# Performance work log

Hardware: AMD Instinct MI355X
Metric: run time of the kernel (lower is better)

## Reference

```python
import jax, jax.numpy as jnp
import numpy as np

NEG_SLOPE = 0.2  # PyG GATConv default negative_slope


def gat_conv(x, edge_index, W, a_src, a_dst, bias, heads, out_ch, concat):
    """PyG-style GATConv (eval mode, add_self_loops=True).
    x: [N, F_in], edge_index: [2, E] (row 0 = src, row 1 = dst).
    """
    N = x.shape[0]
    loop = jnp.arange(N, dtype=edge_index.dtype)
    src = jnp.concatenate([edge_index[0], loop])  # [E+N]
    dst = jnp.concatenate([edge_index[1], loop])

    h = (x @ W).reshape(N, heads, out_ch)            # [N, H, C]
    alpha_s = jnp.einsum('nhc,hc->nh', h, a_src)     # [N, H]
    alpha_d = jnp.einsum('nhc,hc->nh', h, a_dst)

    e = jax.nn.leaky_relu(alpha_s[src] + alpha_d[dst], NEG_SLOPE)  # [E+N, H]
    # softmax over incoming edges per destination node (numerically stable)
    m = jax.ops.segment_max(e, dst, num_segments=N)                # [N, H]
    ex = jnp.exp(e - m[dst])
    denom = jax.ops.segment_sum(ex, dst, num_segments=N)
    alpha = ex / (denom[dst] + 1e-16)                              # [E+N, H]

    msg = h[src] * alpha[:, :, None]                               # [E+N, H, C]
    out = jax.ops.segment_sum(msg, dst, num_segments=N)            # [N, H, C]
    out = out.reshape(N, heads * out_ch) if concat else out.mean(axis=1)
    return out + bias


def setup_inputs() -> dict:
    key = jax.random.key(0)
    ks = jax.random.split(key, 10)
    N, F_in, H, C1, LAT, E = 10000, 2000, 10, 128, 64, 150000
    hid = H * C1  # 1280
    x = jax.random.normal(ks[0], (N, F_in), dtype=jnp.float32)
    edge_index = jax.random.randint(ks[1], (2, E), 0, N, dtype=jnp.int64)
    # layer 1 params (glorot-ish scaling)
    W1 = jax.random.normal(ks[2], (F_in, H * C1), dtype=jnp.float32) * (1.0 / np.sqrt(F_in))
    a_src1 = jax.random.normal(ks[3], (H, C1), dtype=jnp.float32) * 0.1
    a_dst1 = jax.random.normal(ks[4], (H, C1), dtype=jnp.float32) * 0.1
    b1 = jnp.zeros((hid,), dtype=jnp.float32)
    # layer 2 params
    W2 = jax.random.normal(ks[5], (hid, H * LAT), dtype=jnp.float32) * (1.0 / np.sqrt(hid))
    a_src2 = jax.random.normal(ks[6], (H, LAT), dtype=jnp.float32) * 0.1
    a_dst2 = jax.random.normal(ks[7], (H, LAT), dtype=jnp.float32) * 0.1
    b2 = jnp.zeros((LAT,), dtype=jnp.float32)
    return {"x": x, "edge_index": edge_index,
            "W1": W1, "a_src1": a_src1, "a_dst1": a_dst1, "b1": b1,
            "W2": W2, "a_src2": a_src2, "a_dst2": a_dst2, "b2": b2}


def reference(x, edge_index, W1, a_src1, a_dst1, b1, W2, a_src2, a_dst2, b2):
    H, C1, LAT = 10, 128, 64
    h1 = gat_conv(x, edge_index, W1, a_src1, a_dst1, b1, H, C1, concat=True)
    h1 = jax.nn.relu(h1)
    h2 = gat_conv(h1, edge_index, W2, a_src2, a_dst2, b2, H, LAT, concat=False)
    return jax.nn.relu(h2)
```

## Files before the change

### kernel.cpp

```cpp
#include <hip/hip_runtime.h>

#define NN    10000
#define FIN   2000
#define NH    10
#define C1    128
#define C2    64
#define HC1   1280
#define HC2   640
#define MP    10240
#define K1P   2016

typedef _Float16 f16x8 __attribute__((ext_vector_type(8)));
typedef _Float16 f16x4 __attribute__((ext_vector_type(4)));
typedef _Float16 f16x2 __attribute__((ext_vector_type(2)));
typedef float    f32x4 __attribute__((ext_vector_type(4)));

__device__ __forceinline__ float leaky(float x) { return x > 0.f ? x : 0.2f * x; }

__global__ void k_cast_count(const float* __restrict__ src, _Float16* __restrict__ dst,
                             int R, int C4, int Cp4,
                             const int* __restrict__ ei, int* __restrict__ counts, int E) {
    if (blockIdx.x == 1) {
        int e = blockIdx.y * 256 + threadIdx.x;
        if (e < E) atomicAdd(&counts[ei[E + e]], 1);
    }
    int c = blockIdx.x * 256 + threadIdx.x;
    int r = blockIdx.y;
    if (c >= Cp4) return;
    float4 v = make_float4(0.f, 0.f, 0.f, 0.f);
    if (r < R && c < C4) v = *(const float4*)(src + (long)r * (C4 * 4) + 4 * c);
    f16x4 o = {(_Float16)v.x, (_Float16)v.y, (_Float16)v.z, (_Float16)v.w};
    *(f16x4*)(dst + (long)r * (Cp4 * 4) + 4 * c) = o;
}

__global__ void k_transpose_both(const float* __restrict__ W1, _Float16* __restrict__ W1t,
                                 const float* __restrict__ W2, _Float16* __restrict__ W2t,
                                 int* __restrict__ counts) {
    __shared__ float tile[32][33];
    if (blockIdx.x == 0) {
        int i = blockIdx.y * 256 + threadIdx.x;
        if (i <= NN) counts[i] = 0;
    }
    const float* W; _Float16* Wt; int K, N, Kpad, kbase, nbase;
    if (blockIdx.y < 40) {
        W = W1; Wt = W1t; K = FIN; N = HC1; Kpad = K1P;
        kbase = blockIdx.x * 32; nbase = blockIdx.y * 32;
    } else {
        if (blockIdx.x >= 40) return;
        W = W2; Wt = W2t; K = HC1; N = HC2; Kpad = HC1;
        kbase = blockIdx.x * 32; nbase = (blockIdx.y - 40) * 32;
        if (nbase >= N) return;
    }
    int tx = threadIdx.x & 31;
    int ty = threadIdx.x >> 5;
#pragma unroll
    for (int i = 0; i < 4; i++) {
        int k = kbase + ty + i * 8;
        float v = (k < K) ? W[(long)k * N + nbase + tx] : 0.0f;
        tile[ty + i * 8][tx] = v;
    }
    __syncthreads();
#pragma unroll
    for (int i = 0; i < 4; i++) {
        int n = nbase + ty + i * 8;
        Wt[(long)n * Kpad + kbase + tx] = (_Float16)tile[tx][ty + i * 8];
    }
}

__device__ __forceinline__ void gl2lds16(const void* g, void* l) {
    __builtin_amdgcn_global_load_lds((const __attribute__((address_space(1))) void*)g,
                                     (__attribute__((address_space(3))) void*)l, 16, 0, 0);
}

#define WAITCNT_VM6  0x0F76
#define WAITCNT_VM0  0x0F70

__global__ __launch_bounds__(256, 2) void k_gemm(const _Float16* __restrict__ A,
                                                 const _Float16* __restrict__ Bt,
                                                 _Float16* __restrict__ C, int K, int N,
                                                 int NTN,
                                                 const float* __restrict__ asf,
                                                 const float* __restrict__ adf,
                                                 float* __restrict__ as,
                                                 float* __restrict__ ad,
                                                 int headw) {
    __shared__ char smem[73728] __attribute__((aligned(16)));
    _Float16* As = (_Float16*)smem;
    _Float16* Bs = (_Float16*)(smem + 49152);

    int bid = blockIdx.x;
    int r = bid & 7, qb = bid >> 3;
    int n_t = qb % NTN;
    int m_t = r + 8 * (qb / NTN);
    int m0 = m_t * 256;
    int n0 = n_t * 128;
    int t = threadIdx.x;
    int lane = t & 63, wave = t >> 6;
    int wr = wave >> 1, wc = wave & 1;
    int lrow = lane & 15, q = lane >> 4;

    f32x4 acc[8][4] = {};

    int sA[4], sB[2];
#pragma unroll
    for (int i = 0; i < 4; i++) sA[i] = t + 256 * i;
#pragma unroll
    for (int i = 0; i < 2; i++) sB[i] = t + 256 * i;
    const _Float16* Ar[4];
    const _Float16* Br[2];
#pragma unroll
    for (int i = 0; i < 4; i++) {
        int row = sA[i] >> 2, gq = (sA[i] & 3) ^ ((sA[i] >> 3) & 3);
        Ar[i] = A + (long)(m0 + row) * K + gq * 8;
    }
#pragma unroll
    for (int i = 0; i < 2; i++) {
        int row = sB[i] >> 2, gq = (sB[i] & 3) ^ ((sB[i] >> 3) & 3);
        Br[i] = Bt + (long)(n0 + row) * K + gq * 8;
    }

    int aoff[8], boff[4];
#pragma unroll
    for (int i = 0; i < 8; i++) {
        int rowa = wr * 128 + i * 16 + lrow;
        aoff[i] = rowa * 32 + ((q ^ ((rowa >> 1) & 3)) << 3);
    }
#pragma unroll
    for (int i = 0; i < 4; i++) {
        int rowb = wc * 64 + i * 16 + lrow;
        boff[i] = rowb * 32 + ((q ^ ((rowb >> 1) & 3)) << 3);
    }

    auto stage = [&](int it, int buf) {
        int k0 = it << 5;
#pragma unroll
        for (int i = 0; i < 4; i++) gl2lds16(Ar[i] + k0, &As[buf * 8192 + sA[i] * 8]);
#pragma unroll
        for (int i = 0; i < 2; i++) gl2lds16(Br[i] + k0, &Bs[buf * 4096 + sB[i] * 8]);
    };

    int nk = K >> 5;
    stage(0, 0);
    stage(1, 1);
    int cur = 0;
    for (int it = 0; it < nk; it++) {
        if (it + 1 < nk) __builtin_amdgcn_s_waitcnt(WAITCNT_VM6);
        else             __builtin_amdgcn_s_waitcnt(WAITCNT_VM0);
        __builtin_amdgcn_s_barrier();
        int nxt = cur + 2; if (nxt >= 3) nxt -= 3;
        if (it + 2 < nk) stage(it + 2, nxt);

        f16x8 af[8], bf[4];
#pragma unroll
        for (int i = 0; i < 8; i++) af[i] = *(const f16x8*)&As[cur * 8192 + aoff[i]];
#pragma unroll
        for (int i = 0; i < 4; i++) bf[i] = *(const f16x8*)&Bs[cur * 4096 + boff[i]];
#pragma unroll
        for (int mt = 0; mt < 8; mt++)
#pragma unroll
            for (int nt = 0; nt < 4; nt++)
                acc[mt][nt] = __builtin_amdgcn_mfma_f32_16x16x32_f16(bf[nt], af[mt], acc[mt][nt], 0, 0, 0);
        cur = (cur + 1 == 3) ? 0 : cur + 1;
    }

#pragma unroll
    for (int mt = 0; mt < 8; mt++) {
        int m = m0 + wr * 128 + mt * 16 + lrow;
#pragma unroll
        for (int nt = 0; nt < 4; nt++) {
            int n = n0 + wc * 64 + nt * 16 + q * 4;
            f16x4 o = {(_Float16)acc[mt][nt][0], (_Float16)acc[mt][nt][1],
                       (_Float16)acc[mt][nt][2], (_Float16)acc[mt][nt][3]};
            *(f16x4*)(C + (long)m * N + n) = o;
        }
    }

    float4 av[4], dvv[4];
#pragma unroll
    for (int nt = 0; nt < 4; nt++) {
        av[nt]  = *(const float4*)(asf + n0 + wc * 64 + nt * 16 + q * 4);
        dvv[nt] = *(const float4*)(adf + n0 + wc * 64 + nt * 16 + q * 4);
    }
    __syncthreads();
    float* sAs = (float*)smem;
    float* sAd = (float*)smem + 512;
#pragma unroll
    for (int mt = 0; mt < 8; mt++) {
        float ps = 0.f, pd = 0.f;
#pragma unroll
        for (int nt = 0; nt < 4; nt++) {
            ps += acc[mt][nt][0] * av[nt].x + acc[mt][nt][1] * av[nt].y
                + acc[mt][nt][2] * av[nt].z + acc[mt][nt][3] * av[nt].w;
            pd += acc[mt][nt][0] * dvv[nt].x + acc[mt][nt][1] * dvv[nt].y
                + acc[mt][nt][2] * dvv[nt].z + acc[mt][nt][3] * dvv[nt].w;
        }
        ps += __shfl_xor(ps, 16); ps += __shfl_xor(ps, 32);
        pd += __shfl_xor(pd, 16); pd += __shfl_xor(pd, 32);
        if (q == 0) {
            int rl = wr * 128 + mt * 16 + lrow;
            sAs[rl * 2 + wc] = ps;
            sAd[rl * 2 + wc] = pd;
        }
    }
    __syncthreads();
    {
        int m = m0 + t;
        if (m < NN) {
            int hb = n0 / headw;
            if (headw == 128) {
                as[m * NH + hb] = sAs[t * 2] + sAs[t * 2 + 1];
                ad[m * NH + hb] = sAd[t * 2] + sAd[t * 2 + 1];
            } else {
                as[m * NH + hb]     = sAs[t * 2];
                as[m * NH + hb + 1] = sAs[t * 2 + 1];
                ad[m * NH + hb]     = sAd[t * 2];
                ad[m * NH + hb + 1] = sAd[t * 2 + 1];
            }
        }
    }
}

__global__ void k_scan(const int* __restrict__ counts, int* rowptr, int* cursor, int n) {
    __shared__ int s[1024];
    int t = threadIdx.x;
    const int CH = (NN + 1023) / 1024;
    int base = t * CH;
    int loc[CH];
    int sum = 0;
#pragma unroll
    for (int i = 0; i < CH; i++) {
        int idx = base + i;
        int v = (idx < n) ? (counts[idx] + 1) : 0;
        loc[i] = sum;
        sum += v;
    }
    s[t] = sum;
    __syncthreads();
    for (int off = 1; off < 1024; off <<= 1) {
        int add = (t >= off) ? s[t - off] : 0;
        __syncthreads();
        s[t] += add;
        __syncthreads();
    }
    int pre = (t > 0) ? s[t - 1] : 0;
#pragma unroll
    for (int i = 0; i < CH; i++) {
        int idx = base + i;
        if (idx < n) { int ex = pre + loc[i]; rowptr[idx] = ex; cursor[idx] = ex; }
    }
    if (t == 1023) rowptr[n] = s[1023];
}
__global__ void k_csr_fill(const int* __restrict__ ei, int* cursor, int* colidx, int E, int n) {
    int i = blockIdx.x * 256 + threadIdx.x;
    if (i >= E + n) return;
    int s, d;
    if (i < E) { s = ei[i]; d = ei[E + i]; }
    else       { s = i - E; d = i - E; }
    int pos = atomicAdd(&cursor[d], 1);
    colidx[pos] = s;
}

__global__ __launch_bounds__(320) void k_agg1(const int* __restrict__ rowptr,
                                              const int* __restrict__ colidx,
                                              const float* __restrict__ as,
                                              const float* __restrict__ ad,
                                              const _Float16* __restrict__ h,
                                              const float* __restrict__ bias,
                                              _Float16* __restrict__ A2) {
    __shared__ int sidx[64];
    __shared__ float sal[64 * NH];
    int n = blockIdx.x, t = threadIdx.x;
    if (n >= NN) {
        f16x4 z = {(_Float16)0.f, (_Float16)0.f, (_Float16)0.f, (_Float16)0.f};
        *(f16x4*)(A2 + (long)n * HC1 + 4 * t) = z;
        return;
    }
    int k0 = rowptr[n], deg = rowptr[n + 1] - k0;
    int w = t >> 6, lane = t & 63;
    int hd = t >> 5;
    float acc[4] = {0, 0, 0, 0};

    if (deg <= 64) {
        int src = (lane < deg) ? colidx[k0 + lane] : 0;
        float2 adv = *(const float2*)(ad + n * NH + 2 * w);
        float e0 = -1e30f, e1 = -1e30f;
        if (lane < deg) {
            float2 avv = *(const float2*)(as + (long)src * NH + 2 * w);
            e0 = leaky(avv.x + adv.x);
            e1 = leaky(avv.y + adv.y);
        }
        float m0 = e0, m1 = e1;
        for (int m = 32; m; m >>= 1) {
            m0 = fmaxf(m0, __shfl_xor(m0, m));
            m1 = fmaxf(m1, __shfl_xor(m1, m));
        }
        float x0 = (lane < deg) ? __expf(e0 - m0) : 0.f;
        float x1 = (lane < deg) ? __expf(e1 - m1) : 0.f;
        float s0 = x0, s1 = x1;
        for (int m = 32; m; m >>= 1) {
            s0 += __shfl_xor(s0, m);
            s1 += __shfl_xor(s1, m);
        }
        if (lane < deg) {
            sal[lane * NH + 2 * w]     = x0 / (s0 + 1e-16f);
            sal[lane * NH + 2 * w + 1] = x1 / (s1 + 1e-16f);
            if (w == 0) sidx[lane] = src;
        }
        __syncthreads();
        int j = 0;
        for (; j + 4 <= deg; j += 4) {
            int sj0 = sidx[j], sj1 = sidx[j + 1], sj2 = sidx[j + 2], sj3 = sidx[j + 3];
            float a0 = sal[j * NH + hd], a1 = sal[(j + 1) * NH + hd];
            float a2 = sal[(j + 2) * NH + hd], a3 = sal[(j + 3) * NH + hd];
            f16x4 v0 = *(const f16x4*)(h + (long)sj0 * HC1 + 4 * t);
            f16x4 v1 = *(const f16x4*)(h + (long)sj1 * HC1 + 4 * t);
            f16x4 v2 = *(const f16x4*)(h + (long)sj2 * HC1 + 4 * t);
            f16x4 v3 = *(const f16x4*)(h + (long)sj3 * HC1 + 4 * t);
#pragma unroll
            for (int i = 0; i < 4; i++)
                acc[i] += a0 * (float)v0[i] + a1 * (float)v1[i]
                        + a2 * (float)v2[i] + a3 * (float)v3[i];
        }
        for (; j < deg; j++) {
            int src2 = sidx[j];
            float a = sal[j * NH + hd];
            f16x4 v = *(const f16x4*)(h + (long)src2 * HC1 + 4 * t);
#pragma unroll
            for (int i = 0; i < 4; i++) acc[i] += a * (float)v[i];
        }
    } else {
        float2 adv = *(const float2*)(ad + n * NH + 2 * w);
        float m0 = -1e30f, m1 = -1e30f;
        for (int j = lane; j < deg; j += 64) {
            float2 avv = *(const float2*)(as + (long)colidx[k0 + j] * NH + 2 * w);
            m0 = fmaxf(m0, leaky(avv.x + adv.x));
            m1 = fmaxf(m1, leaky(avv.y + adv.y));
        }
        for (int m = 32; m; m >>= 1) {
            m0 = fmaxf(m0, __shfl_xor(m0, m));
            m1 = fmaxf(m1, __shfl_xor(m1, m));
        }
        float s0 = 0.f, s1 = 0.f;
        for (int j = lane; j < deg; j += 64) {
            float2 avv = *(const float2*)(as + (long)colidx[k0 + j] * NH + 2 * w);
            s0 += __expf(leaky(avv.x + adv.x) - m0);
            s1 += __expf(leaky(avv.y + adv.y) - m1);
        }
        for (int m = 32; m; m >>= 1) {
            s0 += __shfl_xor(s0, m);
            s1 += __shfl_xor(s1, m);
        }
        float i0 = 1.f / (s0 + 1e-16f), i1 = 1.f / (s1 + 1e-16f);
        for (int c0 = 0; c0 < deg; c0 += 64) {
            int cn = min(64, deg - c0);
            __syncthreads();
            if (lane < cn) {
                int src = colidx[k0 + c0 + lane];
                float2 avv = *(const float2*)(as + (long)src * NH + 2 * w);
                sal[lane * NH + 2 * w]     = __expf(leaky(avv.x + adv.x) - m0) * i0;
                sal[lane * NH + 2 * w + 1] = __expf(leaky(avv.y + adv.y) - m1) * i1;
                if (w == 0) sidx[lane] = src;
            }
            __syncthreads();
            for (int j = 0; j < cn; j++) {
                int src2 = sidx[j];
                float a = sal[j * NH + hd];
                f16x4 v = *(const f16x4*)(h + (long)src2 * HC1 + 4 * t);
#pragma unroll
                for (int i = 0; i < 4; i++) acc[i] += a * (float)v[i];
            }
        }
    }
    f16x4 o;
#pragma unroll
    for (int i = 0; i < 4; i++) {
        float x = acc[i] + bias[4 * t + i];
        o[i] = (_Float16)(x > 0.f ? x : 0.f);
    }
    *(f16x4*)(A2 + (long)n * HC1 + 4 * t) = o;
}

__global__ __launch_bounds__(320) void k_agg2(const int* __restrict__ rowptr,
                                              const int* __restrict__ colidx,
                                              const float* __restrict__ as,
                                              const float* __restrict__ ad,
                                              const _Float16* __restrict__ h,
                                              const float* __restrict__ bias,
                                              float* __restrict__ out) {
    __shared__ int sidx[64];
    __shared__ float sal[64 * NH];
    __shared__ float facc[HC2];
    int n = blockIdx.x, t = threadIdx.x;
    int k0 = rowptr[n], deg = rowptr[n + 1] - k0;
    int w = t >> 6, lane = t & 63;
    int hd = t >> 5;
    float a0 = 0.f, a1 = 0.f;

    if (deg <= 64) {
        int src = (lane < deg) ? colidx[k0 + lane] : 0;
        float2 adv = *(const float2*)(ad + n * NH + 2 * w);
        float e0 = -1e30f, e1 = -1e30f;
        if (lane < deg) {
            float2 avv = *(const float2*)(as + (long)src * NH + 2 * w);
            e0 = leaky(avv.x + adv.x);
            e1 = leaky(avv.y + adv.y);
        }
        float m0 = e0, m1 = e1;
        for (int m = 32; m; m >>= 1) {
            m0 = fmaxf(m0, __shfl_xor(m0, m));
            m1 = fmaxf(m1, __shfl_xor(m1, m));
        }
        float x0 = (lane < deg) ? __expf(e0 - m0) : 0.f;
        float x1 = (lane < deg) ? __expf(e1 - m1) : 0.f;
        float s0 = x0, s1 = x1;
        for (int m = 32; m; m >>= 1) {
            s0 += __shfl_xor(s0, m);
            s1 += __shfl_xor(s1, m);
        }
        if (lane < deg) {
            sal[lane * NH + 2 * w]     = x0 / (s0 + 1e-16f);
            sal[lane * NH + 2 * w + 1] = x1 / (s1 + 1e-16f);
            if (w == 0) sidx[lane] = src;
        }
        __syncthreads();
        int j = 0;
        for (; j + 4 <= deg; j += 4) {
            int sj0 = sidx[j], sj1 = sidx[j + 1], sj2 = sidx[j + 2], sj3 = sidx[j + 3];
            float b0 = sal[j * NH + hd], b1 = sal[(j + 1) * NH + hd];
            float b2 = sal[(j + 2) * NH + hd], b3 = sal[(j + 3) * NH + hd];
            f16x2 v0 = *(const f16x2*)(h + (long)sj0 * HC2 + 2 * t);
            f16x2 v1 = *(const f16x2*)(h + (long)sj1 * HC2 + 2 * t);
            f16x2 v2 = *(const f16x2*)(h + (long)sj2 * HC2 + 2 * t);
            f16x2 v3 = *(const f16x2*)(h + (long)sj3 * HC2 + 2 * t);
            a0 += b0 * (float)v0[0] + b1 * (float)v1[0] + b2 * (float)v2[0] + b3 * (float)v3[0];
            a1 += b0 * (float)v0[1] + b1 * (float)v1[1] + b2 * (float)v2[1] + b3 * (float)v3[1];
        }
        for (; j < deg; j++) {
            int src2 = sidx[j];
            float a = sal[j * NH + hd];
            f16x2 v = *(const f16x2*)(h + (long)src2 * HC2 + 2 * t);
            a0 += a * (float)v[0];
            a1 += a * (float)v[1];
        }
    } else {
        float2 adv = *(const float2*)(ad + n * NH + 2 * w);
        float m0 = -1e30f, m1 = -1e30f;
        for (int j = lane; j < deg; j += 64) {
            float2 avv = *(const float2*)(as + (long)colidx[k0 + j] * NH + 2 * w);
            m0 = fmaxf(m0, leaky(avv.x + adv.x));
            m1 = fmaxf(m1, leaky(avv.y + adv.y));
        }
        for (int m = 32; m; m >>= 1) {
            m0 = fmaxf(m0, __shfl_xor(m0, m));
            m1 = fmaxf(m1, __shfl_xor(m1, m));
        }
        float s0 = 0.f, s1 = 0.f;
        for (int j = lane; j < deg; j += 64) {
            float2 avv = *(const float2*)(as + (long)colidx[k0 + j] * NH + 2 * w);
            s0 += __expf(leaky(avv.x + adv.x) - m0);
            s1 += __expf(leaky(avv.y + adv.y) - m1);
        }
        for (int m = 32; m; m >>= 1) {
            s0 += __shfl_xor(s0, m);
            s1 += __shfl_xor(s1, m);
        }
        float i0 = 1.f / (s0 + 1e-16f), i1 = 1.f / (s1 + 1e-16f);
        for (int c0 = 0; c0 < deg; c0 += 64) {
            int cn = min(64, deg - c0);
            __syncthreads();
            if (lane < cn) {
                int src = colidx[k0 + c0 + lane];
                float2 avv = *(const float2*)(as + (long)src * NH + 2 * w);
                sal[lane * NH + 2 * w]     = __expf(leaky(avv.x + adv.x) - m0) * i0;
                sal[lane * NH + 2 * w + 1] = __expf(leaky(avv.y + adv.y) - m1) * i1;
                if (w == 0) sidx[lane] = src;
            }
            __syncthreads();
            for (int j = 0; j < cn; j++) {
                int src2 = sidx[j];
                float a = sal[j * NH + hd];
                f16x2 v = *(const f16x2*)(h + (long)src2 * HC2 + 2 * t);
                a0 += a * (float)v[0];
                a1 += a * (float)v[1];
            }
        }
    }
    facc[2 * t] = a0;
    facc[2 * t + 1] = a1;
    __syncthreads();
    if (t < C2) {
        float s = 0.f;
#pragma unroll
        for (int hh = 0; hh < NH; hh++) s += facc[hh * C2 + t];
        s = s * 0.1f + bias[t];
        out[(long)n * C2 + t] = s > 0.f ? s : 0.f;
    }
}

extern "C" void kernel_launch(void* const* d_in, const int* in_sizes, int n_in,
                              void* d_out, int out_size, void* d_ws, size_t ws_size,
                              hipStream_t stream) {
    const float* x      = (const float*)d_in[0];
    const int*   ei     = (const int*)d_in[1];
    const float* W1     = (const float*)d_in[2];
    const float* asrc1  = (const float*)d_in[3];
    const float* adst1  = (const float*)d_in[4];
    const float* b1     = (const float*)d_in[5];
    const float* W2     = (const float*)d_in[6];
    const float* asrc2  = (const float*)d_in[7];
    const float* adst2  = (const float*)d_in[8];
    const float* b2     = (const float*)d_in[9];
    float* out = (float*)d_out;
    const int E  = in_sizes[1] / 2;
    const int EN = E + NN;

    char* base = (char*)d_ws;
    size_t o = 0;
    auto alloc = [&](size_t bytes) { size_t r = o; o += (bytes + 255) & ~(size_t)255; return r; };
    _Float16* A1    = (_Float16*)(base + alloc((size_t)MP * K1P * 2));
    _Float16* W1t   = (_Float16*)(base + alloc((size_t)HC1 * K1P * 2));
    _Float16* A2    = (_Float16*)(base + alloc((size_t)MP * HC1 * 2));
    _Float16* W2t   = (_Float16*)(base + alloc((size_t)HC2 * HC1 * 2));
    _Float16* h1pre = (_Float16*)(base + alloc((size_t)MP * HC1 * 2));
    _Float16* h2pre = (_Float16*)(base + alloc((size_t)MP * HC2 * 2));
    float* as1      = (float*)(base + alloc((size_t)NN * NH * 4));
    float* ad1      = (float*)(base + alloc((size_t)NN * NH * 4));
    float* as2      = (float*)(base + alloc((size_t)NN * NH * 4));
    float* ad2      = (float*)(base + alloc((size_t)NN * NH * 4));
    int* counts     = (int*)(base + alloc((size_t)(NN + 1) * 4));
    int* rowptr     = (int*)(base + alloc((size_t)(NN + 1) * 4));
    int* cursor     = (int*)(base + alloc((size_t)(NN + 1) * 4));
    int* colidx     = (int*)(base + alloc((size_t)EN * 4));
    (void)ws_size; (void)n_in; (void)out_size;

    k_transpose_both<<<dim3(63, 60), 256, 0, stream>>>(W1, W1t, W2, W2t, counts);
    k_cast_count<<<dim3(2, MP), 256, 0, stream>>>(x, A1, NN, FIN / 4, K1P / 4, ei, counts, E);
    k_gemm<<<8 * (MP / 256 / 8) * (HC1 / 128), 256, 0, stream>>>(A1, W1t, h1pre, K1P, HC1, HC1 / 128,
                                                                 asrc1, adst1, as1, ad1, C1);
    k_scan<<<1, 1024, 0, stream>>>(counts, rowptr, cursor, NN);
    k_csr_fill<<<(EN + 255) / 256, 256, 0, stream>>>(ei, cursor, colidx, E, NN);
    k_agg1<<<MP, 320, 0, stream>>>(rowptr, colidx, as1, ad1, h1pre, b1, A2);
    k_gemm<<<8 * (MP / 256 / 8) * (HC2 / 128), 256, 0, stream>>>(A2, W2t, h2pre, HC1, HC2, HC2 / 128,
                                                                 asrc2, adst2, as2, ad2, C2);
    k_agg2<<<NN, 320, 0, stream>>>(rowptr, colidx, as2, ad2, h2pre, b2, out);
}
```

Baseline: 379.3 us.

## Merge prep kernels, fold CSR fill into GEMM1 grid, shrink GEMM2 M-tile

Merges the cast, weight-transpose and degree-count kernels into one flat-grid prep kernel, and replaces the in-kernel counts zeroing with a memset. The CSR fill now runs as extra blocks appended to the first GEMM grid, so it overlaps with the GEMM instead of needing its own launch. The GEMM is templated on M-fragment count so the second, smaller GEMM uses 128-row tiles and launches more blocks, improving CU fill. The cost is fewer launches and better occupancy, in exchange for more complex control flow and atomic traffic that shares the GEMM's time window.

```diff
diff --git a/kernel.cpp b/kernel.cpp
--- a/kernel.cpp
+++ b/kernel.cpp
@@ -17,42 +17,40 @@
 
 __device__ __forceinline__ float leaky(float x) { return x > 0.f ? x : 0.2f * x; }
 
-__global__ void k_cast_count(const float* __restrict__ src, _Float16* __restrict__ dst,
-                             int R, int C4, int Cp4,
-                             const int* __restrict__ ei, int* __restrict__ counts, int E) {
-    if (blockIdx.x == 1) {
-        int e = blockIdx.y * 256 + threadIdx.x;
+#define NCAST (2 * MP)
+#define NW1   (63 * 40)
+#define NW2   (40 * 20)
+__global__ void k_prep(const float* __restrict__ x, _Float16* __restrict__ A1,
+                       const float* __restrict__ W1, _Float16* __restrict__ W1t,
+                       const float* __restrict__ W2, _Float16* __restrict__ W2t,
+                       const int* __restrict__ ei, int* __restrict__ counts, int E) {
+    __shared__ float tile[32][33];
+    int bid = blockIdx.x, t = threadIdx.x;
+    if (bid < NCAST) {
+        int r = bid >> 1;
+        int c = (bid & 1) * 256 + t;
+        if (c >= K1P / 4) return;
+        float4 v = make_float4(0.f, 0.f, 0.f, 0.f);
+        if (r < NN && c < FIN / 4) v = *(const float4*)(x + (long)r * FIN + 4 * c);
+        f16x4 o = {(_Float16)v.x, (_Float16)v.y, (_Float16)v.z, (_Float16)v.w};
+        *(f16x4*)(A1 + (long)r * K1P + 4 * c) = o;
+        return;
+    }
+    const float* W; _Float16* Wt; int K, N, Kpad, kbase, nbase;
+    if (bid < NCAST + NW1) {
+        int i = bid - NCAST;
+        W = W1; Wt = W1t; K = FIN; N = HC1; Kpad = K1P;
+        kbase = (i % 63) * 32; nbase = (i / 63) * 32;
+    } else if (bid < NCAST + NW1 + NW2) {
+        int i = bid - NCAST - NW1;
+        W = W2; Wt = W2t; K = HC1; N = HC2; Kpad = HC1;
+        kbase = (i % 40) * 32; nbase = (i / 40) * 32;
+    } else {
+        int e = (bid - NCAST - NW1 - NW2) * 256 + t;
         if (e < E) atomicAdd(&counts[ei[E + e]], 1);
-    }
-    int c = blockIdx.x * 256 + threadIdx.x;
-    int r = blockIdx.y;
-    if (c >= Cp4) return;
-    float4 v = make_float4(0.f, 0.f, 0.f, 0.f);
-    if (r < R && c < C4) v = *(const float4*)(src + (long)r * (C4 * 4) + 4 * c);
-    f16x4 o = {(_Float16)v.x, (_Float16)v.y, (_Float16)v.z, (_Float16)v.w};
-    *(f16x4*)(dst + (long)r * (Cp4 * 4) + 4 * c) = o;
-}
-
-__global__ void k_transpose_both(const float* __restrict__ W1, _Float16* __restrict__ W1t,
-                                 const float* __restrict__ W2, _Float16* __restrict__ W2t,
-                                 int* __restrict__ counts) {
-    __shared__ float tile[32][33];
-    if (blockIdx.x == 0) {
-        int i = blockIdx.y * 256 + threadIdx.x;
-        if (i <= NN) counts[i] = 0;
-    }
-    const float* W; _Float16* Wt; int K, N, Kpad, kbase, nbase;
-    if (blockIdx.y < 40) {
-        W = W1; Wt = W1t; K = FIN; N = HC1; Kpad = K1P;
-        kbase = blockIdx.x * 32; nbase = blockIdx.y * 32;
-    } else {
-        if (blockIdx.x >= 40) return;
-        W = W2; Wt = W2t; K = HC1; N = HC2; Kpad = HC1;
-        kbase = blockIdx.x * 32; nbase = (blockIdx.y - 40) * 32;
-        if (nbase >= N) return;
-    }
-    int tx = threadIdx.x & 31;
-    int ty = threadIdx.x >> 5;
+        return;
+    }
+    int tx = t & 31, ty = t >> 5;
 #pragma unroll
     for (int i = 0; i < 4; i++) {
         int k = kbase + ty + i * 8;
@@ -72,9 +70,7 @@
                                      (__attribute__((address_space(3))) void*)l, 16, 0, 0);
 }
 
-#define WAITCNT_VM6  0x0F76
-#define WAITCNT_VM0  0x0F70
-
+template<int MFRAG>
 __global__ __launch_bounds__(256, 2) void k_gemm(const _Float16* __restrict__ A,
                                                  const _Float16* __restrict__ Bt,
                                                  _Float16* __restrict__ C, int K, int N,
@@ -83,33 +79,51 @@
                                                  const float* __restrict__ adf,
                                                  float* __restrict__ as,
                                                  float* __restrict__ ad,
-                                                 int headw) {
-    __shared__ char smem[73728] __attribute__((aligned(16)));
+                                                 int headw, int nblk,
+                                                 const int* __restrict__ ei,
+                                                 int* __restrict__ cursor,
+                                                 int* __restrict__ colidx, int E) {
+    constexpr int BM   = MFRAG * 32;
+    constexpr int ABUF = BM * 32;
+    constexpr int ASL  = BM / 64;
+    constexpr int WVM  = 0x0F70 | (ASL + 2);
+    __shared__ char smem[3 * ABUF * 2 + 3 * 8192] __attribute__((aligned(16)));
     _Float16* As = (_Float16*)smem;
-    _Float16* Bs = (_Float16*)(smem + 49152);
+    _Float16* Bs = (_Float16*)(smem + 3 * ABUF * 2);
 
     int bid = blockIdx.x;
+    if (bid >= nblk) {
+        int i = (bid - nblk) * 256 + threadIdx.x;
+        if (i < E + NN) {
+            int s, d;
+            if (i < E) { s = ei[i]; d = ei[E + i]; }
+            else       { s = i - E; d = i - E; }
+            int pos = atomicAdd(&cursor[d], 1);
+            colidx[pos] = s;
+        }
+        return;
+    }
     int r = bid & 7, qb = bid >> 3;
     int n_t = qb % NTN;
     int m_t = r + 8 * (qb / NTN);
-    int m0 = m_t * 256;
+    int m0 = m_t * BM;
     int n0 = n_t * 128;
     int t = threadIdx.x;
     int lane = t & 63, wave = t >> 6;
     int wr = wave >> 1, wc = wave & 1;
     int lrow = lane & 15, q = lane >> 4;
 
-    f32x4 acc[8][4] = {};
-
-    int sA[4], sB[2];
-#pragma unroll
-    for (int i = 0; i < 4; i++) sA[i] = t + 256 * i;
+    f32x4 acc[MFRAG][4] = {};
+
+    int sA[ASL], sB[2];
+#pragma unroll
+    for (int i = 0; i < ASL; i++) sA[i] = t + 256 * i;
 #pragma unroll
     for (int i = 0; i < 2; i++) sB[i] = t + 256 * i;
-    const _Float16* Ar[4];
+    const _Float16* Ar[ASL];
     const _Float16* Br[2];
 #pragma unroll
-    for (int i = 0; i < 4; i++) {
+    for (int i = 0; i < ASL; i++) {
         int row = sA[i] >> 2, gq = (sA[i] & 3) ^ ((sA[i] >> 3) & 3);
         Ar[i] = A + (long)(m0 + row) * K + gq * 8;
     }
@@ -119,10 +133,10 @@
         Br[i] = Bt + (long)(n0 + row) * K + gq * 8;
     }
 
-    int aoff[8], boff[4];
-#pragma unroll
-    for (int i = 0; i < 8; i++) {
-        int rowa = wr * 128 + i * 16 + lrow;
+    int aoff[MFRAG], boff[4];
+#pragma unroll
+    for (int i = 0; i < MFRAG; i++) {
+        int rowa = wr * (MFRAG * 16) + i * 16 + lrow;
         aoff[i] = rowa * 32 + ((q ^ ((rowa >> 1) & 3)) << 3);
     }
 #pragma unroll
@@ -134,7 +148,7 @@
     auto stage = [&](int it, int buf) {
         int k0 = it << 5;
 #pragma unroll
-        for (int i = 0; i < 4; i++) gl2lds16(Ar[i] + k0, &As[buf * 8192 + sA[i] * 8]);
+        for (int i = 0; i < ASL; i++) gl2lds16(Ar[i] + k0, &As[buf * ABUF + sA[i] * 8]);
 #pragma unroll
         for (int i = 0; i < 2; i++) gl2lds16(Br[i] + k0, &Bs[buf * 4096 + sB[i] * 8]);
     };
@@ -144,19 +158,19 @@
     stage(1, 1);
     int cur = 0;
     for (int it = 0; it < nk; it++) {
-        if (it + 1 < nk) __builtin_amdgcn_s_waitcnt(WAITCNT_VM6);
-        else             __builtin_amdgcn_s_waitcnt(WAITCNT_VM0);
+        if (it + 1 < nk) __builtin_amdgcn_s_waitcnt(WVM);
+        else             __builtin_amdgcn_s_waitcnt(0x0F70);
         __builtin_amdgcn_s_barrier();
         int nxt = cur + 2; if (nxt >= 3) nxt -= 3;
         if (it + 2 < nk) stage(it + 2, nxt);
 
-        f16x8 af[8], bf[4];
-#pragma unroll
-        for (int i = 0; i < 8; i++) af[i] = *(const f16x8*)&As[cur * 8192 + aoff[i]];
+        f16x8 af[MFRAG], bf[4];
+#pragma unroll
+        for (int i = 0; i < MFRAG; i++) af[i] = *(const f16x8*)&As[cur * ABUF + aoff[i]];
 #pragma unroll
         for (int i = 0; i < 4; i++) bf[i] = *(const f16x8*)&Bs[cur * 4096 + boff[i]];
 #pragma unroll
-        for (int mt = 0; mt < 8; mt++)
+        for (int mt = 0; mt < MFRAG; mt++)
 #pragma unroll
             for (int nt = 0; nt < 4; nt++)
                 acc[mt][nt] = __builtin_amdgcn_mfma_f32_16x16x32_f16(bf[nt], af[mt], acc[mt][nt], 0, 0, 0);
@@ -164,8 +178,8 @@
     }
 
 #pragma unroll
-    for (int mt = 0; mt < 8; mt++) {
-        int m = m0 + wr * 128 + mt * 16 + lrow;
+    for (int mt = 0; mt < MFRAG; mt++) {
+        int m = m0 + wr * (MFRAG * 16) + mt * 16 + lrow;
 #pragma unroll
         for (int nt = 0; nt < 4; nt++) {
             int n = n0 + wc * 64 + nt * 16 + q * 4;
@@ -183,9 +197,9 @@
     }
     __syncthreads();
     float* sAs = (float*)smem;
-    float* sAd = (float*)smem + 512;
-#pragma unroll
-    for (int mt = 0; mt < 8; mt++) {
+    float* sAd = (float*)smem + BM * 2;
+#pragma unroll
+    for (int mt = 0; mt < MFRAG; mt++) {
         float ps = 0.f, pd = 0.f;
 #pragma unroll
         for (int nt = 0; nt < 4; nt++) {
@@ -197,13 +211,13 @@
         ps += __shfl_xor(ps, 16); ps += __shfl_xor(ps, 32);
         pd += __shfl_xor(pd, 16); pd += __shfl_xor(pd, 32);
         if (q == 0) {
-            int rl = wr * 128 + mt * 16 + lrow;
+            int rl = wr * (MFRAG * 16) + mt * 16 + lrow;
             sAs[rl * 2 + wc] = ps;
             sAd[rl * 2 + wc] = pd;
         }
     }
     __syncthreads();
-    {
+    if (t < BM) {
         int m = m0 + t;
         if (m < NN) {
             int hb = n0 / headw;
@@ -249,15 +263,6 @@
         if (idx < n) { int ex = pre + loc[i]; rowptr[idx] = ex; cursor[idx] = ex; }
     }
     if (t == 1023) rowptr[n] = s[1023];
-}
-__global__ void k_csr_fill(const int* __restrict__ ei, int* cursor, int* colidx, int E, int n) {
-    int i = blockIdx.x * 256 + threadIdx.x;
-    if (i >= E + n) return;
-    int s, d;
-    if (i < E) { s = ei[i]; d = ei[E + i]; }
-    else       { s = i - E; d = i - E; }
-    int pos = atomicAdd(&cursor[d], 1);
-    colidx[pos] = s;
 }
 
 __global__ __launch_bounds__(320) void k_agg1(const int* __restrict__ rowptr,
@@ -533,14 +538,20 @@
     int* colidx     = (int*)(base + alloc((size_t)EN * 4));
     (void)ws_size; (void)n_in; (void)out_size;
 
-    k_transpose_both<<<dim3(63, 60), 256, 0, stream>>>(W1, W1t, W2, W2t, counts);
-    k_cast_count<<<dim3(2, MP), 256, 0, stream>>>(x, A1, NN, FIN / 4, K1P / 4, ei, counts, E);
-    k_gemm<<<8 * (MP / 256 / 8) * (HC1 / 128), 256, 0, stream>>>(A1, W1t, h1pre, K1P, HC1, HC1 / 128,
-                                                                 asrc1, adst1, as1, ad1, C1);
+    const int NCNT = (E + 255) / 256;
+    const int FILLB = (EN + 255) / 256;
+    const int G1 = 8 * (MP / 256 / 8) * (HC1 / 128);
+    const int G2 = 8 * (MP / 128 / 8) * (HC2 / 128);
+
+    hipMemsetAsync(counts, 0, (size_t)(NN + 1) * 4, stream);
+    k_prep<<<NCAST + NW1 + NW2 + NCNT, 256, 0, stream>>>(x, A1, W1, W1t, W2, W2t, ei, counts, E);
     k_scan<<<1, 1024, 0, stream>>>(counts, rowptr, cursor, NN);
-    k_csr_fill<<<(EN + 255) / 256, 256, 0, stream>>>(ei, cursor, colidx, E, NN);
+    k_gemm<8><<<G1 + FILLB, 256, 0, stream>>>(A1, W1t, h1pre, K1P, HC1, HC1 / 128,
+                                              asrc1, adst1, as1, ad1, C1,
+                                              G1, ei, cursor, colidx, E);
     k_agg1<<<MP, 320, 0, stream>>>(rowptr, colidx, as1, ad1, h1pre, b1, A2);
-    k_gemm<<<8 * (MP / 256 / 8) * (HC2 / 128), 256, 0, stream>>>(A2, W2t, h2pre, HC1, HC2, HC2 / 128,
-                                                                 asrc2, adst2, as2, ad2, C2);
+    k_gemm<4><<<G2, 256, 0, stream>>>(A2, W2t, h2pre, HC1, HC2, HC2 / 128,
+                                      asrc2, adst2, as2, ad2, C2,
+                                      G2, ei, cursor, colidx, E);
     k_agg2<<<NN, 320, 0, stream>>>(rowptr, colidx, as2, ad2, h2pre, b2, out);
 }
```

Measured after the change: 363.2 us. 4.3% less time.
